# Optimization experiments

Measured on AMD Instinct MI355X. Metric: run time of the kernel, lower is better.

The kernel has to match this reference:

```python
import jax, jax.numpy as jnp
import numpy as np

TEMPERATURE = 0.5
EPS = 1e-8  # torch CosineSimilarity eps


def setup_inputs() -> dict:
    key = jax.random.key(0)
    k1, k2 = jax.random.split(key)
    B, D = 4096, 256
    return {
        "z_i": jax.random.normal(k1, (B, D), dtype=jnp.float32),
        "z_j": jax.random.normal(k2, (B, D), dtype=jnp.float32),
    }


def reference(z_i, z_j):
    B = z_i.shape[0]
    N = 2 * B
    z = jnp.concatenate([z_i, z_j], axis=0)  # [N, D]
    # cosine similarity == normalized dot product (eps-clamped norms like torch)
    norms = jnp.maximum(jnp.linalg.norm(z, axis=1, keepdims=True), EPS)
    zn = z / norms
    sim = jnp.matmul(zn, zn.T) / TEMPERATURE  # [N, N]

    idx = jnp.arange(B)
    # positives: diag(sim, +B) and diag(sim, -B)
    pos = jnp.concatenate([sim[idx, idx + B], sim[idx + B, idx]])  # [N]

    # CrossEntropy with label 0 over [pos_i, negatives_i] reduces to
    # logsumexp over row i excluding the self-diagonal, minus pos_i.
    r = jnp.arange(N)
    neg_inf = jnp.finfo(sim.dtype).min
    sim_masked = jnp.where(r[:, None] == r[None, :], neg_inf, sim)
    lse = jax.nn.logsumexp(sim_masked, axis=1)  # [N]

    loss = (jnp.sum(lse) - jnp.sum(pos)) / N
    return loss
```

## Files before the change

### kernel.cpp

```cpp
#include <hip/hip_runtime.h>
#include <cstdint>

#define B_ROWS 4096
#define N_ROWS 8192
#define D_DIM  256
#define BT     128
#define TGRID  64
#define NTILES 2080
#define NKT    4

typedef __attribute__((ext_vector_type(4))) float f32x4;
typedef __attribute__((ext_vector_type(2))) unsigned long u64x2;

__device__ __forceinline__ void gload16(const void* g, void* l) {
    __builtin_amdgcn_global_load_lds(
        (const __attribute__((address_space(1))) void*)g,
        (__attribute__((address_space(3))) void*)l, 16, 0, 0);
}

__device__ __forceinline__ f32x4 exp4(f32x4 v) {
    f32x4 r;
    r.x = __expf(v.x); r.y = __expf(v.y); r.z = __expf(v.z); r.w = __expf(v.w);
    return r;
}

__device__ __forceinline__ unsigned f2e4m3(float f) {
    union { float f; unsigned u; } v; v.f = f;
    unsigned s = (v.u >> 24) & 0x80u;
    unsigned mag = v.u & 0x7fffffffu;
    int e = (int)(mag >> 23) - 127;
    if (e >= -6) {
        unsigned r = mag + 0x7ffffu + ((mag >> 20) & 1u);
        int e2 = (int)(r >> 23) - 127;
        unsigned m3 = (r >> 20) & 7u;
        return s | (unsigned)((e2 + 7) << 3) | m3;
    }
    if (e < -10) return s;
    float q = rintf(fabsf(f) * 512.0f);
    unsigned qi = (unsigned)q;
    return s | qi;
}

__global__ __launch_bounds__(256) void normpos_kernel(const float* __restrict__ zi,
                                                      const float* __restrict__ zj,
                                                      unsigned char* __restrict__ zn,
                                                      float* __restrict__ pospartial) {
    int wid = threadIdx.x >> 6;
    int lane = threadIdx.x & 63;
    int p = blockIdx.x * 4 + wid;
    f32x4 ga = *(const f32x4*)(zi + (size_t)p * D_DIM + lane * 4);
    f32x4 gb = *(const f32x4*)(zj + (size_t)p * D_DIM + lane * 4);
    float sa = ga.x * ga.x + ga.y * ga.y + ga.z * ga.z + ga.w * ga.w;
    float sb = gb.x * gb.x + gb.y * gb.y + gb.z * gb.z + gb.w * gb.w;
    #pragma unroll
    for (int m = 1; m < 64; m <<= 1) { sa += __shfl_xor(sa, m, 64); sb += __shfl_xor(sb, m, 64); }
    float fa = 1.41421356237309515f / fmaxf(sqrtf(sa), 1e-8f);
    float fb = 1.41421356237309515f / fmaxf(sqrtf(sb), 1e-8f);
    f32x4 na, nb;
    na.x = ga.x * fa; na.y = ga.y * fa; na.z = ga.z * fa; na.w = ga.w * fa;
    nb.x = gb.x * fb; nb.y = gb.y * fb; nb.z = gb.z * fb; nb.w = gb.w * fb;
    unsigned pa = f2e4m3(na.x) | (f2e4m3(na.y) << 8) | (f2e4m3(na.z) << 16) | (f2e4m3(na.w) << 24);
    unsigned pb = f2e4m3(nb.x) | (f2e4m3(nb.y) << 8) | (f2e4m3(nb.z) << 16) | (f2e4m3(nb.w) << 24);
    int bytepos = (lane >> 4) * 64 + ((lane >> 1) & 3) * 16 + ((lane >> 3) & 1) * 8 + 4 * (lane & 1);
    *(unsigned*)(zn + (size_t)p * 256 + bytepos) = pa;
    *(unsigned*)(zn + (size_t)(p + B_ROWS) * 256 + bytepos) = pb;
    float d = na.x * nb.x + na.y * nb.y + na.z * nb.z + na.w * nb.w;
    #pragma unroll
    for (int m = 1; m < 64; m <<= 1) d += __shfl_xor(d, m, 64);
    if (lane == 0) pospartial[p] = d;
}

__global__ __launch_bounds__(256) void simclr_gemm_kernel(const unsigned char* __restrict__ zn,
                                                          float* __restrict__ P) {
    __shared__ unsigned char As[BT * 64];
    __shared__ unsigned char Bs[BT * 64];
    __shared__ float rPpart[2][BT];
    __shared__ float cPpart[2][BT];

    const int tid = threadIdx.x;
    const int lane = tid & 63, wid = tid >> 6;
    const int wr = wid >> 1, wc = wid & 1;

    int bid = (int)((blockIdx.x & 7) * (NTILES / 8) + (blockIdx.x >> 3));
    int ti = (int)((129.0f - sqrtf(16641.0f - 8.0f * (float)bid)) * 0.5f);
    while ((ti + 1) * TGRID - ((ti + 1) * ti) / 2 <= bid) ++ti;
    while (ti * TGRID - (ti * (ti - 1)) / 2 > bid) --ti;
    const int tj = ti + (bid - (ti * TGRID - (ti * (ti - 1)) / 2));

    const char* gA = (const char*)zn + (size_t)ti * BT * 256;
    const char* gB = (const char*)zn + (size_t)tj * BT * 256;

    const int r0 = tid >> 2;
    const int sch = (tid & 3) ^ ((tid >> 3) & 3);
    const size_t gof0 = (size_t)r0 * 256 + (size_t)sch * 16;
    const size_t gof1 = (size_t)(64 + r0) * 256 + (size_t)sch * 16;
    const unsigned lo0 = (unsigned)tid * 16;
    const unsigned lo1 = 4096u + (unsigned)tid * 16;

    f32x4 acc[4][4];
    #pragma unroll
    for (int m = 0; m < 4; ++m)
        #pragma unroll
        for (int n = 0; n < 4; ++n)
            acc[m][n] = (f32x4){0.f, 0.f, 0.f, 0.f};

    const int ysw = (lane >> 4) ^ (((lane & 15) >> 1) & 3);
    const int arow = wr * 64 + (lane & 15);
    const int brow = wc * 64 + (lane & 15);

    #pragma unroll
    for (int kt = 0; kt < NKT; ++kt) {
        const size_t kb = (size_t)kt * 64;
        gload16(gA + gof0 + kb, &As[lo0]);
        gload16(gA + gof1 + kb, &As[lo1]);
        gload16(gB + gof0 + kb, &Bs[lo0]);
        gload16(gB + gof1 + kb, &Bs[lo1]);
        __syncthreads();

        u64x2 af[4], bfr[4];
        #pragma unroll
        for (int m = 0; m < 4; ++m)
            af[m] = *(const u64x2*)&As[(arow + m * 16) * 64 + ysw * 16];
        #pragma unroll
        for (int n = 0; n < 4; ++n)
            bfr[n] = *(const u64x2*)&Bs[(brow + n * 16) * 64 + ysw * 16];

        #pragma unroll
        for (int m = 0; m < 4; ++m)
            #pragma unroll
            for (int n = 0; n < 4; ++n) {
                acc[m][n] = __builtin_amdgcn_mfma_f32_16x16x32_fp8_fp8(
                    (long)af[m].x, (long)bfr[n].x, acc[m][n], 0, 0, 0);
                acc[m][n] = __builtin_amdgcn_mfma_f32_16x16x32_fp8_fp8(
                    (long)af[m].y, (long)bfr[n].y, acc[m][n], 0, 0, 0);
            }
        __syncthreads();
    }

    float cs[4] = {0.f, 0.f, 0.f, 0.f};
    #pragma unroll
    for (int m = 0; m < 4; ++m) {
        f32x4 ef[4];
        #pragma unroll
        for (int n = 0; n < 4; ++n) ef[n] = exp4(acc[m][n]);
        f32x4 rv = ef[0] + ef[1] + ef[2] + ef[3];
        #pragma unroll
        for (int msk = 1; msk <= 8; msk <<= 1) {
            rv.x += __shfl_xor(rv.x, msk, 64);
            rv.y += __shfl_xor(rv.y, msk, 64);
            rv.z += __shfl_xor(rv.z, msk, 64);
            rv.w += __shfl_xor(rv.w, msk, 64);
        }
        if ((lane & 15) == 0) {
            int rbase = wr * 64 + m * 16 + (lane >> 4) * 4;
            rPpart[wc][rbase + 0] = rv.x;
            rPpart[wc][rbase + 1] = rv.y;
            rPpart[wc][rbase + 2] = rv.z;
            rPpart[wc][rbase + 3] = rv.w;
        }
        #pragma unroll
        for (int n = 0; n < 4; ++n)
            cs[n] += ef[n].x + ef[n].y + ef[n].z + ef[n].w;
    }
    #pragma unroll
    for (int n = 0; n < 4; ++n) {
        float c = cs[n];
        c += __shfl_xor(c, 16, 64);
        c += __shfl_xor(c, 32, 64);
        if (lane < 16) cPpart[wr][wc * 64 + n * 16 + lane] = c;
    }
    __syncthreads();

    if (tid < BT) {
        P[(size_t)tj * N_ROWS + ti * BT + tid] = rPpart[0][tid] + rPpart[1][tid];
    } else if (ti != tj) {
        int t = tid - BT;
        P[(size_t)ti * N_ROWS + tj * BT + t] = cPpart[0][t] + cPpart[1][t];
    }
}

__global__ __launch_bounds__(128) void reduce_rows_kernel(const float* __restrict__ P,
                                                          const float* __restrict__ pospartial,
                                                          float* __restrict__ blockpart) {
    const float E2 = 7.38905609893065f;
    int row = blockIdx.x * 128 + threadIdx.x;
    float s = 0.f;
    #pragma unroll 16
    for (int src = 0; src < TGRID; ++src)
        s += P[(size_t)src * N_ROWS + row];
    float v = logf(s - E2);
    if (row < B_ROWS) v -= 2.0f * pospartial[row];
    #pragma unroll
    for (int m = 1; m < 64; m <<= 1) v += __shfl_xor(v, m, 64);
    __shared__ float ws[2];
    if ((threadIdx.x & 63) == 0) ws[threadIdx.x >> 6] = v;
    __syncthreads();
    if (threadIdx.x == 0) blockpart[blockIdx.x] = ws[0] + ws[1];
}

__global__ __launch_bounds__(64) void final_kernel(const float* __restrict__ blockpart,
                                                   float* __restrict__ out) {
    int lane = threadIdx.x;
    float v = blockpart[lane];
    #pragma unroll
    for (int m = 1; m < 64; m <<= 1) v += __shfl_xor(v, m, 64);
    if (lane == 0) out[0] = v / (float)N_ROWS;
}

extern "C" void kernel_launch(void* const* d_in, const int* in_sizes, int n_in,
                              void* d_out, int out_size, void* d_ws, size_t ws_size,
                              hipStream_t stream) {
    const float* zi = (const float*)d_in[0];
    const float* zj = (const float*)d_in[1];
    char* ws = (char*)d_ws;
    unsigned char* zn = (unsigned char*)ws;
    float* P = (float*)(ws + 2 * 1024 * 1024);
    float* pospartial = (float*)(ws + 4 * 1024 * 1024);
    float* blockpart = (float*)(ws + 4 * 1024 * 1024 + 16 * 1024);

    normpos_kernel<<<B_ROWS / 4, 256, 0, stream>>>(zi, zj, zn, pospartial);
    simclr_gemm_kernel<<<NTILES, 256, 0, stream>>>(zn, P);
    reduce_rows_kernel<<<N_ROWS / 128, 128, 0, stream>>>(P, pospartial, blockpart);
    final_kernel<<<1, 64, 0, stream>>>(blockpart, (float*)d_out);
}
```

Measured before the change: 38.77 us.

## Enlarge GEMM tiles to 256x256 with 512 threads and K-step 128

Doubles the symmetric-GEMM tile from 128 to 256 rows, uses 8 waves per block, and halves the K loop to two steps of 128 bytes with a new XOR swizzle. The number of upper-triangular tiles drops from 2080 to 528, so operand reloads and partial-sum writes shrink. The P partial buffer is re-indexed (row partials in slots 0-31, column partials in 32-63), and the reduction kernel is changed to pick the matching slot per row segment. In exchange, the larger tile uses 64KB of LDS and more registers per block, and 528 blocks may fill the CUs less evenly.

New measurement: 47.45 us. +22.4%, slower.

```diff
diff --git a/kernel.cpp b/kernel.cpp
--- a/kernel.cpp
+++ b/kernel.cpp
@@ -4,10 +4,9 @@
 #define B_ROWS 4096
 #define N_ROWS 8192
 #define D_DIM  256
-#define BT     128
-#define TGRID  64
-#define NTILES 2080
-#define NKT    4
+#define BT     256
+#define TG     32
+#define NTILES 528
 
 typedef __attribute__((ext_vector_type(4))) float f32x4;
 typedef __attribute__((ext_vector_type(2))) unsigned long u64x2;
@@ -70,76 +69,78 @@
     if (lane == 0) pospartial[p] = d;
 }
 
-__global__ __launch_bounds__(256) void simclr_gemm_kernel(const unsigned char* __restrict__ zn,
+__global__ __launch_bounds__(512) void simclr_gemm_kernel(const unsigned char* __restrict__ zn,
                                                           float* __restrict__ P) {
-    __shared__ unsigned char As[BT * 64];
-    __shared__ unsigned char Bs[BT * 64];
-    __shared__ float rPpart[2][BT];
+    __shared__ unsigned char As[32768];
+    __shared__ unsigned char Bs[32768];
+    __shared__ float rPpart[4][BT];
     __shared__ float cPpart[2][BT];
 
     const int tid = threadIdx.x;
     const int lane = tid & 63, wid = tid >> 6;
-    const int wr = wid >> 1, wc = wid & 1;
+    const int wr = wid >> 2, wc = wid & 3;
+    const int l15 = lane & 15, lq = lane >> 4;
 
     int bid = (int)((blockIdx.x & 7) * (NTILES / 8) + (blockIdx.x >> 3));
-    int ti = (int)((129.0f - sqrtf(16641.0f - 8.0f * (float)bid)) * 0.5f);
-    while ((ti + 1) * TGRID - ((ti + 1) * ti) / 2 <= bid) ++ti;
-    while (ti * TGRID - (ti * (ti - 1)) / 2 > bid) --ti;
-    const int tj = ti + (bid - (ti * TGRID - (ti * (ti - 1)) / 2));
+    int ti = (int)((65.0f - sqrtf(4225.0f - 8.0f * (float)bid)) * 0.5f);
+    if (ti > 31) ti = 31;
+    while (ti < 31 && (ti + 1) * TG - ((ti + 1) * ti) / 2 <= bid) ++ti;
+    while (ti > 0 && ti * TG - (ti * (ti - 1)) / 2 > bid) --ti;
+    const int tj = ti + (bid - (ti * TG - (ti * (ti - 1)) / 2));
 
     const char* gA = (const char*)zn + (size_t)ti * BT * 256;
     const char* gB = (const char*)zn + (size_t)tj * BT * 256;
 
-    const int r0 = tid >> 2;
-    const int sch = (tid & 3) ^ ((tid >> 3) & 3);
-    const size_t gof0 = (size_t)r0 * 256 + (size_t)sch * 16;
-    const size_t gof1 = (size_t)(64 + r0) * 256 + (size_t)sch * 16;
-    const unsigned lo0 = (unsigned)tid * 16;
-    const unsigned lo1 = 4096u + (unsigned)tid * 16;
-
-    f32x4 acc[4][4];
-    #pragma unroll
-    for (int m = 0; m < 4; ++m)
+    const int rr = tid >> 3;
+    const int us = (tid & 7) ^ (rr & 7);
+    const unsigned lo = (unsigned)tid * 16;
+
+    f32x4 acc[8][4];
+    #pragma unroll
+    for (int m = 0; m < 8; ++m)
         #pragma unroll
         for (int n = 0; n < 4; ++n)
             acc[m][n] = (f32x4){0.f, 0.f, 0.f, 0.f};
 
-    const int ysw = (lane >> 4) ^ (((lane & 15) >> 1) & 3);
-    const int arow = wr * 64 + (lane & 15);
-    const int brow = wc * 64 + (lane & 15);
-
-    #pragma unroll
-    for (int kt = 0; kt < NKT; ++kt) {
-        const size_t kb = (size_t)kt * 64;
-        gload16(gA + gof0 + kb, &As[lo0]);
-        gload16(gA + gof1 + kb, &As[lo1]);
-        gload16(gB + gof0 + kb, &Bs[lo0]);
-        gload16(gB + gof1 + kb, &Bs[lo1]);
+    const int arow = wr * 128 + l15;
+    const int brow = wc * 64 + l15;
+    const int x7 = l15 & 7;
+
+    #pragma unroll
+    for (int kt = 0; kt < 2; ++kt) {
+        #pragma unroll
+        for (int q = 0; q < 4; ++q) {
+            size_t go = (size_t)(q * 64 + rr) * 256 + (size_t)kt * 128 + (size_t)us * 16;
+            gload16(gA + go, &As[q * 8192 + lo]);
+            gload16(gB + go, &Bs[q * 8192 + lo]);
+        }
         __syncthreads();
 
-        u64x2 af[4], bfr[4];
-        #pragma unroll
-        for (int m = 0; m < 4; ++m)
-            af[m] = *(const u64x2*)&As[(arow + m * 16) * 64 + ysw * 16];
-        #pragma unroll
-        for (int n = 0; n < 4; ++n)
-            bfr[n] = *(const u64x2*)&Bs[(brow + n * 16) * 64 + ysw * 16];
-
-        #pragma unroll
-        for (int m = 0; m < 4; ++m)
+        #pragma unroll
+        for (int gp = 0; gp < 2; ++gp) {
+            const int slotb = ((gp * 4 + lq) ^ x7) * 16;
+            u64x2 bfr[4];
             #pragma unroll
-            for (int n = 0; n < 4; ++n) {
-                acc[m][n] = __builtin_amdgcn_mfma_f32_16x16x32_fp8_fp8(
-                    (long)af[m].x, (long)bfr[n].x, acc[m][n], 0, 0, 0);
-                acc[m][n] = __builtin_amdgcn_mfma_f32_16x16x32_fp8_fp8(
-                    (long)af[m].y, (long)bfr[n].y, acc[m][n], 0, 0, 0);
+            for (int n = 0; n < 4; ++n)
+                bfr[n] = *(const u64x2*)&Bs[(brow + n * 16) * 128 + slotb];
+            #pragma unroll
+            for (int m = 0; m < 8; ++m) {
+                u64x2 af = *(const u64x2*)&As[(arow + m * 16) * 128 + slotb];
+                #pragma unroll
+                for (int n = 0; n < 4; ++n) {
+                    acc[m][n] = __builtin_amdgcn_mfma_f32_16x16x32_fp8_fp8(
+                        (long)af.x, (long)bfr[n].x, acc[m][n], 0, 0, 0);
+                    acc[m][n] = __builtin_amdgcn_mfma_f32_16x16x32_fp8_fp8(
+                        (long)af.y, (long)bfr[n].y, acc[m][n], 0, 0, 0);
+                }
             }
+        }
         __syncthreads();
     }
 
     float cs[4] = {0.f, 0.f, 0.f, 0.f};
     #pragma unroll
-    for (int m = 0; m < 4; ++m) {
+    for (int m = 0; m < 8; ++m) {
         f32x4 ef[4];
         #pragma unroll
         for (int n = 0; n < 4; ++n) ef[n] = exp4(acc[m][n]);
@@ -151,8 +152,8 @@
             rv.z += __shfl_xor(rv.z, msk, 64);
             rv.w += __shfl_xor(rv.w, msk, 64);
         }
-        if ((lane & 15) == 0) {
-            int rbase = wr * 64 + m * 16 + (lane >> 4) * 4;
+        if (l15 == 0) {
+            int rbase = wr * 128 + m * 16 + lq * 4;
             rPpart[wc][rbase + 0] = rv.x;
             rPpart[wc][rbase + 1] = rv.y;
             rPpart[wc][rbase + 2] = rv.z;
@@ -172,10 +173,11 @@
     __syncthreads();
 
     if (tid < BT) {
-        P[(size_t)tj * N_ROWS + ti * BT + tid] = rPpart[0][tid] + rPpart[1][tid];
+        P[(size_t)tj * N_ROWS + (size_t)ti * BT + tid] =
+            rPpart[0][tid] + rPpart[1][tid] + rPpart[2][tid] + rPpart[3][tid];
     } else if (ti != tj) {
         int t = tid - BT;
-        P[(size_t)ti * N_ROWS + tj * BT + t] = cPpart[0][t] + cPpart[1][t];
+        P[(size_t)(32 + ti) * N_ROWS + (size_t)tj * BT + t] = cPpart[0][t] + cPpart[1][t];
     }
 }
 
@@ -184,10 +186,13 @@
                                                           float* __restrict__ blockpart) {
     const float E2 = 7.38905609893065f;
     int row = blockIdx.x * 128 + threadIdx.x;
+    int seg = row >> 8;
     float s = 0.f;
-    #pragma unroll 16
-    for (int src = 0; src < TGRID; ++src)
+    #pragma unroll 8
+    for (int k = 0; k < TG; ++k) {
+        int src = (k >= seg) ? k : (32 + k);
         s += P[(size_t)src * N_ROWS + row];
+    }
     float v = logf(s - E2);
     if (row < B_ROWS) v -= 2.0f * pospartial[row];
     #pragma unroll
@@ -219,7 +224,7 @@
     float* blockpart = (float*)(ws + 4 * 1024 * 1024 + 16 * 1024);
 
     normpos_kernel<<<B_ROWS / 4, 256, 0, stream>>>(zi, zj, zn, pospartial);
-    simclr_gemm_kernel<<<NTILES, 256, 0, stream>>>(zn, P);
+    simclr_gemm_kernel<<<NTILES, 512, 0, stream>>>(zn, P);
     reduce_rows_kernel<<<N_ROWS / 128, 128, 0, stream>>>(P, pospartial, blockpart);
     final_kernel<<<1, 64, 0, stream>>>(blockpart, (float*)d_out);
 }
```
